# Optimization experiments

Measured on AMD Instinct MI355X. Metric: run time of the kernel, lower is better.

Reference implementation:

```python
import jax, jax.numpy as jnp
import numpy as np

B, W, N, L = 64, 256, 128, 64


def setup_inputs() -> dict:
    key = jax.random.key(0)
    k1, k2, k3 = jax.random.split(key, 3)
    x = jax.random.normal(k1, (B, W, L), dtype=jnp.float32)
    shapelets = jax.random.normal(k2, (N, L), dtype=jnp.float32)
    cls_w = jax.random.normal(k3, (1, N), dtype=jnp.float32) * 0.1
    cls_b = jnp.zeros((1,), dtype=jnp.float32)
    return {"x": x, "shapelets": shapelets, "cls_w": cls_w, "cls_b": cls_b}


def reference(x, shapelets, cls_w, cls_b):
    # diffs: [B, W, N, L] broadcast subtract
    diffs = x[:, :, None, :] - shapelets[None, None, :, :]
    # L2 norm over shapelet-length axis -> [B, W, N]
    discrim = jnp.sqrt(jnp.sum(diffs * diffs, axis=3))
    # min over windows -> [B, N]
    min_discrim = jnp.min(discrim, axis=1)
    # tiny classifier: Linear(N, 1) + sigmoid -> [B, 1]
    logits = min_discrim @ cls_w.T + cls_b
    return jax.nn.sigmoid(logits)
```

## Files before the change

kernel.cpp:

```cpp
#include <hip/hip_runtime.h>
#include <cfloat>
#include <cmath>

constexpr int B = 64;
constexpr int W = 256;
constexpr int N = 128;
constexpr int L = 64;

template <int NCHUNKS>
__global__ __launch_bounds__(256) void shapelet_min_kernel(
    const float* __restrict__ x, const float* __restrict__ shp,
    float* __restrict__ part) {
  constexpr int WPB = W / NCHUNKS;
  __shared__ float xs[WPB * L];

  const int blk = blockIdx.x;
  const int b = blk / NCHUNKS;
  const int c = blk % NCHUNKS;
  const int tid = threadIdx.x;
  const int n = tid & (N - 1);
  const int wslot = tid >> 7;

  {
    const float4* xg =
        (const float4*)(x + (size_t)b * W * L + (size_t)c * WPB * L);
    float4* xls = (float4*)xs;
    constexpr int NV4 = WPB * L / 4;
    for (int i = tid; i < NV4; i += 256) xls[i] = xg[i];
  }

  float s[L];
  {
    const float4* sg = (const float4*)(shp + (size_t)n * L);
#pragma unroll
    for (int i = 0; i < L / 4; ++i) {
      float4 v = sg[i];
      s[4 * i + 0] = v.x;
      s[4 * i + 1] = v.y;
      s[4 * i + 2] = v.z;
      s[4 * i + 3] = v.w;
    }
  }

  __syncthreads();

  float best = FLT_MAX;
  const int w0 = wslot * (WPB / 2);
  for (int wi = 0; wi < WPB / 2; ++wi) {
    const float* xr = xs + (size_t)(w0 + wi) * L;
    float a0 = 0.f, a1 = 0.f, a2 = 0.f, a3 = 0.f;
#pragma unroll
    for (int l = 0; l < L; l += 4) {
      float4 xv = *(const float4*)(xr + l);
      float d0 = xv.x - s[l + 0]; a0 = fmaf(d0, d0, a0);
      float d1 = xv.y - s[l + 1]; a1 = fmaf(d1, d1, a1);
      float d2 = xv.z - s[l + 2]; a2 = fmaf(d2, d2, a2);
      float d3 = xv.w - s[l + 3]; a3 = fmaf(d3, d3, a3);
    }
    best = fminf(best, (a0 + a1) + (a2 + a3));
  }

  __syncthreads();
  if (wslot == 1) xs[n] = best;
  __syncthreads();
  if (wslot == 0) {
    part[((size_t)b * NCHUNKS + c) * N + n] = fminf(best, xs[n]);
  }
}

template <int NCHUNKS>
__global__ __launch_bounds__(128) void shapelet_head_kernel(
    const float* __restrict__ part, const float* __restrict__ cls_w,
    const float* __restrict__ cls_b, float* __restrict__ out) {
  const int b = blockIdx.x;
  const int n = threadIdx.x;

  float m = FLT_MAX;
#pragma unroll
  for (int c = 0; c < NCHUNKS; ++c)
    m = fminf(m, part[((size_t)b * NCHUNKS + c) * N + n]);

  float v = sqrtf(m) * cls_w[n];

#pragma unroll
  for (int off = 32; off > 0; off >>= 1) v += __shfl_down(v, off, 64);

  __shared__ float red[2];
  if ((n & 63) == 0) red[n >> 6] = v;
  __syncthreads();
  if (n == 0) {
    float z = red[0] + red[1] + cls_b[0];
    out[b] = 1.0f / (1.0f + expf(-z));
  }
}

template <int NCHUNKS>
static void launch_impl(const float* x, const float* shp, const float* cls_w,
                        const float* cls_b, float* out, float* part,
                        hipStream_t stream) {
  shapelet_min_kernel<NCHUNKS>
      <<<B * NCHUNKS, 256, 0, stream>>>(x, shp, part);
  shapelet_head_kernel<NCHUNKS>
      <<<B, 128, 0, stream>>>(part, cls_w, cls_b, out);
}

extern "C" void kernel_launch(void* const* d_in, const int* in_sizes, int n_in,
                              void* d_out, int out_size, void* d_ws,
                              size_t ws_size, hipStream_t stream) {
  const float* x = (const float*)d_in[0];
  const float* shp = (const float*)d_in[1];
  const float* cls_w = (const float*)d_in[2];
  const float* cls_b = (const float*)d_in[3];
  float* out = (float*)d_out;
  float* part = (float*)d_ws;

  const size_t per_chunk = (size_t)B * N * sizeof(float);
  if (ws_size >= 8 * per_chunk) {
    launch_impl<8>(x, shp, cls_w, cls_b, out, part, stream);
  } else if (ws_size >= 4 * per_chunk) {
    launch_impl<4>(x, shp, cls_w, cls_b, out, part, stream);
  } else if (ws_size >= 2 * per_chunk) {
    launch_impl<2>(x, shp, cls_w, cls_b, out, part, stream);
  } else {
    launch_impl<1>(x, shp, cls_w, cls_b, out, part, stream);
  }
}
```

Before: 76.81 us.

## Expand squared distance into norms minus twice dot product and add 16-chunk split

```diff
diff --git a/kernel.cpp b/kernel.cpp
--- a/kernel.cpp
+++ b/kernel.cpp
@@ -12,21 +12,39 @@
     const float* __restrict__ x, const float* __restrict__ shp,
     float* __restrict__ part) {
   constexpr int WPB = W / NCHUNKS;
+  constexpr int NV4 = WPB * L / 4;
   __shared__ float xs[WPB * L];
+  __shared__ float xnorm_s[WPB];
+  __shared__ float comb[N];
 
-  const int blk = blockIdx.x;
-  const int b = blk / NCHUNKS;
-  const int c = blk % NCHUNKS;
+  const int b = blockIdx.x / NCHUNKS;
+  const int c = blockIdx.x % NCHUNKS;
   const int tid = threadIdx.x;
   const int n = tid & (N - 1);
   const int wslot = tid >> 7;
 
-  {
-    const float4* xg =
-        (const float4*)(x + (size_t)b * W * L + (size_t)c * WPB * L);
-    float4* xls = (float4*)xs;
-    constexpr int NV4 = WPB * L / 4;
-    for (int i = tid; i < NV4; i += 256) xls[i] = xg[i];
+  const float4* xg =
+      (const float4*)(x + ((size_t)b * W + (size_t)c * WPB) * L);
+  float4* xls = (float4*)xs;
+
+  if constexpr (NV4 == 256) {
+    float4 v = xg[tid];
+    xls[tid] = v;
+    float p = v.x * v.x + v.y * v.y + v.z * v.z + v.w * v.w;
+    p += __shfl_xor(p, 8, 16);
+    p += __shfl_xor(p, 4, 16);
+    p += __shfl_xor(p, 2, 16);
+    p += __shfl_xor(p, 1, 16);
+    if ((tid & 15) == 0) xnorm_s[tid >> 4] = p;
+  } else {
+    if (tid < WPB) xnorm_s[tid] = 0.f;
+    __syncthreads();
+    for (int i = tid; i < NV4; i += 256) {
+      float4 v = xg[i];
+      xls[i] = v;
+      float p = v.x * v.x + v.y * v.y + v.z * v.z + v.w * v.w;
+      atomicAdd(&xnorm_s[i >> 4], p);
+    }
   }
 
   float s[L];
@@ -52,26 +70,28 @@
 #pragma unroll
     for (int l = 0; l < L; l += 4) {
       float4 xv = *(const float4*)(xr + l);
-      float d0 = xv.x - s[l + 0]; a0 = fmaf(d0, d0, a0);
-      float d1 = xv.y - s[l + 1]; a1 = fmaf(d1, d1, a1);
-      float d2 = xv.z - s[l + 2]; a2 = fmaf(d2, d2, a2);
-      float d3 = xv.w - s[l + 3]; a3 = fmaf(d3, d3, a3);
+      a0 = fmaf(xv.x, s[l + 0], a0);
+      a1 = fmaf(xv.y, s[l + 1], a1);
+      a2 = fmaf(xv.z, s[l + 2], a2);
+      a3 = fmaf(xv.w, s[l + 3], a3);
     }
-    best = fminf(best, (a0 + a1) + (a2 + a3));
+    float dot = (a0 + a1) + (a2 + a3);
+    best = fminf(best, fmaf(-2.f, dot, xnorm_s[w0 + wi]));
   }
 
   __syncthreads();
-  if (wslot == 1) xs[n] = best;
+  if (wslot == 1) comb[n] = best;
   __syncthreads();
   if (wslot == 0) {
-    part[((size_t)b * NCHUNKS + c) * N + n] = fminf(best, xs[n]);
+    part[((size_t)b * NCHUNKS + c) * N + n] = fminf(best, comb[n]);
   }
 }
 
 template <int NCHUNKS>
 __global__ __launch_bounds__(128) void shapelet_head_kernel(
-    const float* __restrict__ part, const float* __restrict__ cls_w,
-    const float* __restrict__ cls_b, float* __restrict__ out) {
+    const float* __restrict__ part, const float* __restrict__ shp,
+    const float* __restrict__ cls_w, const float* __restrict__ cls_b,
+    float* __restrict__ out) {
   const int b = blockIdx.x;
   const int n = threadIdx.x;
 
@@ -80,7 +100,21 @@
   for (int c = 0; c < NCHUNKS; ++c)
     m = fminf(m, part[((size_t)b * NCHUNKS + c) * N + n]);
 
-  float v = sqrtf(m) * cls_w[n];
+  float sn = 0.f;
+  {
+    const float4* sg = (const float4*)(shp + (size_t)n * L);
+#pragma unroll
+    for (int i = 0; i < L / 4; ++i) {
+      float4 v = sg[i];
+      sn = fmaf(v.x, v.x, sn);
+      sn = fmaf(v.y, v.y, sn);
+      sn = fmaf(v.z, v.z, sn);
+      sn = fmaf(v.w, v.w, sn);
+    }
+  }
+
+  float d2 = fmaxf(m + sn, 0.f);
+  float v = sqrtf(d2) * cls_w[n];
 
 #pragma unroll
   for (int off = 32; off > 0; off >>= 1) v += __shfl_down(v, off, 64);
@@ -98,10 +132,9 @@
 static void launch_impl(const float* x, const float* shp, const float* cls_w,
                         const float* cls_b, float* out, float* part,
                         hipStream_t stream) {
-  shapelet_min_kernel<NCHUNKS>
-      <<<B * NCHUNKS, 256, 0, stream>>>(x, shp, part);
+  shapelet_min_kernel<NCHUNKS><<<B * NCHUNKS, 256, 0, stream>>>(x, shp, part);
   shapelet_head_kernel<NCHUNKS>
-      <<<B, 128, 0, stream>>>(part, cls_w, cls_b, out);
+      <<<B, 128, 0, stream>>>(part, shp, cls_w, cls_b, out);
 }
 
 extern "C" void kernel_launch(void* const* d_in, const int* in_sizes, int n_in,
@@ -115,12 +148,12 @@
   float* part = (float*)d_ws;
 
   const size_t per_chunk = (size_t)B * N * sizeof(float);
-  if (ws_size >= 8 * per_chunk) {
+  if (ws_size >= 16 * per_chunk) {
+    launch_impl<16>(x, shp, cls_w, cls_b, out, part, stream);
+  } else if (ws_size >= 8 * per_chunk) {
     launch_impl<8>(x, shp, cls_w, cls_b, out, part, stream);
   } else if (ws_size >= 4 * per_chunk) {
     launch_impl<4>(x, shp, cls_w, cls_b, out, part, stream);
-  } else if (ws_size >= 2 * per_chunk) {
-    launch_impl<2>(x, shp, cls_w, cls_b, out, part, stream);
   } else {
     launch_impl<1>(x, shp, cls_w, cls_b, out, part, stream);
   }
```

Result: faster. 71.84 us (-6.5%).
